# Performance work log

Hardware: AMD Instinct MI355X
Metric: run time of the kernel (lower is better)

Reference implementation:

```python
import jax, jax.numpy as jnp
import numpy as np

DIM = 1024
SCALE = 1.0 / np.sqrt(DIM).astype(np.float32)


def setup_inputs() -> dict:
    key = jax.random.key(0)
    ks = jax.random.split(key, 8)
    B, S, D = 4, 2048, DIM
    x = jax.random.normal(ks[0], (B, S, D), dtype=jnp.float32)
    mask = jnp.zeros((S, S), dtype=jnp.float32)  # additive mask, broadcast over batch
    # learned params (nn.Linear: y = x @ W.T + b); store W already transposed for x @ W
    init = 1.0 / np.sqrt(D)
    Wq = jax.random.uniform(ks[1], (D, D), jnp.float32, -init, init)
    bq = jax.random.uniform(ks[2], (D,), jnp.float32, -init, init)
    Wk = jax.random.uniform(ks[3], (D, D), jnp.float32, -init, init)
    bk = jax.random.uniform(ks[4], (D,), jnp.float32, -init, init)
    Wv = jax.random.uniform(ks[5], (D, D), jnp.float32, -init, init)
    bv = jax.random.uniform(ks[6], (D,), jnp.float32, -init, init)
    return {"x": x, "mask": mask, "Wq": Wq, "bq": bq, "Wk": Wk, "bk": bk, "Wv": Wv, "bv": bv}


def reference(x, mask, Wq, bq, Wk, bk, Wv, bv):
    # single-head full-dim attention, scaled by 1/sqrt(dim) (as in the source)
    q = x @ Wq + bq                      # [B, S, D]
    k = x @ Wk + bk                      # [B, S, D]
    v = x @ Wv + bv                      # [B, S, D]
    scores = jnp.einsum('bqd,bkd->bqk', q, k) * SCALE  # [B, S, S]
    scores = scores + mask               # additive mask, broadcast
    attn = jax.nn.softmax(scores, axis=-1)
    # dropout(p=0.1) is identity in eval mode
    return jnp.einsum('bqk,bkd->bqd', attn, v)  # [B, S, D]
```

## Files before the change

kernel.cpp:

```cpp
#include <hip/hip_runtime.h>

typedef unsigned short u16;
typedef unsigned int u32;

typedef __attribute__((ext_vector_type(8))) short bf16x8;
typedef __attribute__((ext_vector_type(4))) float f32x4;

static __device__ __forceinline__ u16 f2bf(float f) {
    u32 u = __float_as_uint(f);
    u32 r = (u + 0x7FFFu + ((u >> 16) & 1u)) >> 16;
    return (u16)r;
}
static __device__ __forceinline__ float bf2f(u16 h) {
    return __uint_as_float(((u32)h) << 16);
}
static __device__ __forceinline__ u32 pack2(float a, float b) {
    return (u32)f2bf(a) | ((u32)f2bf(b) << 16);
}

__global__ __launch_bounds__(256) void convert_bf16_kernel(const float* __restrict__ x,
                                                           u16* __restrict__ y, int n4) {
    int i = blockIdx.x * 256 + threadIdx.x;
    if (i < n4) {
        float4 v = ((const float4*)x)[i];
        ushort4 o;
        o.x = f2bf(v.x); o.y = f2bf(v.y); o.z = f2bf(v.z); o.w = f2bf(v.w);
        ((ushort4*)y)[i] = o;
    }
}

__global__ __launch_bounds__(256) void transpose_to_bf16_kernel(const float* __restrict__ W,
                                                                u16* __restrict__ WT, int D) {
    __shared__ float t[32][33];
    int bx = blockIdx.x, by = blockIdx.y;
    int tx = threadIdx.x, ty = threadIdx.y;
#pragma unroll
    for (int i = ty; i < 32; i += 8)
        t[i][tx] = W[(long)(by * 32 + i) * D + bx * 32 + tx];
    __syncthreads();
#pragma unroll
    for (int i = ty; i < 32; i += 8)
        WT[(long)(bx * 32 + i) * D + by * 32 + tx] = f2bf(t[tx][i]);
}

__global__ __launch_bounds__(256) void concat_bias_kernel(const float* __restrict__ a,
                                                          const float* __restrict__ b,
                                                          float* __restrict__ o, int n) {
    int i = blockIdx.x * 256 + threadIdx.x;
    if (i < 2 * n) o[i] = (i < n) ? a[i] : b[i - n];
}


__global__ __launch_bounds__(512, 4) void gemm_wide_kernel(
    const u16* __restrict__ A, int lda, long sA,
    const u16* __restrict__ B, int ldb, long sB,
    void* __restrict__ C, int ldc, long sC, int c_bf16,
    const float* __restrict__ bias, int bias_mode,
    const float* __restrict__ madd, int mask_ld,
    float scale, int K) {
    __shared__ __align__(16) u16 SMEM[2][384 * 32];
    const int bz = blockIdx.z;
    const u16* Ab = A + (long)bz * sA;
    const u16* Bb = B + (long)bz * sB;
    const int tm = blockIdx.y * 256, tn = blockIdx.x * 128;
    const int tid = threadIdx.x, wave = tid >> 6, lane = tid & 63;
    const int wm = (wave & 3) * 64, wn = (wave >> 2) * 64;
    const int lr = lane >> 2, c = lane & 3;
    const int fm = lane & 15, fq = lane >> 4;

    f32x4 acc[4][4];
#pragma unroll
    for (int i = 0; i < 4; i++)
#pragma unroll
        for (int j = 0; j < 4; j++) acc[i][j] = (f32x4){0.f, 0.f, 0.f, 0.f};

    const int T = K >> 5;

    auto stage = [&](int t, int buf) {
        u16* As = &SMEM[buf][0];
        u16* Bs = &SMEM[buf][256 * 32];
#pragma unroll
        for (int r = 0; r < 2; r++) {
            const int rl = wave * 32 + r * 16;
            const int row = rl + lr;
            const int kc = (t << 5) + ((c ^ ((row ^ (row >> 2)) & 3)) << 3);
            const u16* ga = Ab + (long)(tm + row) * lda + kc;
            __builtin_amdgcn_global_load_lds((const __attribute__((address_space(1))) void*)ga,
                                             (__attribute__((address_space(3))) void*)&As[rl * 32],
                                             16, 0, 0);
        }
        {
            const int rl = wave * 16;
            const int row = rl + lr;
            const int kc = (t << 5) + ((c ^ ((row ^ (row >> 2)) & 3)) << 3);
            const u16* gb = Bb + (long)(tn + row) * ldb + kc;
            __builtin_amdgcn_global_load_lds((const __attribute__((address_space(1))) void*)gb,
                                             (__attribute__((address_space(3))) void*)&Bs[rl * 32],
                                             16, 0, 0);
        }
    };

    stage(0, 0);
    __syncthreads();
    for (int t = 0; t < T; t++) {
        const int cur = t & 1;
        if (t + 1 < T) stage(t + 1, cur ^ 1);
        const u16* As = &SMEM[cur][0];
        const u16* Bs = &SMEM[cur][256 * 32];
        bf16x8 af[4], bfr[4];
#pragma unroll
        for (int i = 0; i < 4; i++) {
            int row = wm + i * 16 + fm;
            af[i] = *(const bf16x8*)&As[row * 32 + ((fq ^ ((row ^ (row >> 2)) & 3)) << 3)];
        }
#pragma unroll
        for (int j = 0; j < 4; j++) {
            int row = wn + j * 16 + fm;
            bfr[j] = *(const bf16x8*)&Bs[row * 32 + ((fq ^ ((row ^ (row >> 2)) & 3)) << 3)];
        }
#pragma unroll
        for (int i = 0; i < 4; i++)
#pragma unroll
            for (int j = 0; j < 4; j++)
                acc[i][j] = __builtin_amdgcn_mfma_f32_16x16x32_bf16(af[i], bfr[j], acc[i][j], 0, 0, 0);
        if (t + 1 < T) __syncthreads();
    }
    __syncthreads();

    float* EP = (float*)&SMEM[0][0] + wave * 1088;
    const int row16 = lane >> 2, cb = (lane & 3) * 16;
    float4 bc[4];
    if (bias_mode == 1) {
#pragma unroll
        for (int q = 0; q < 4; q++) bc[q] = *(const float4*)&bias[tn + wn + cb + q * 4];
    }
#pragma unroll
    for (int i = 0; i < 4; i++) {
#pragma unroll
        for (int j = 0; j < 4; j++)
#pragma unroll
            for (int r = 0; r < 4; r++)
                EP[(fq * 4 + r) * 68 + j * 16 + fm] = acc[i][j][r];
        const long grow = tm + wm + i * 16 + row16;
        float rb = (bias_mode == 2) ? bias[grow] : 0.f;
        float4 t4[4];
#pragma unroll
        for (int q = 0; q < 4; q++) {
            float4 v = *(const float4*)&EP[row16 * 68 + cb + q * 4];
            v.x = v.x * scale + rb; v.y = v.y * scale + rb;
            v.z = v.z * scale + rb; v.w = v.w * scale + rb;
            if (bias_mode == 1) { v.x += bc[q].x; v.y += bc[q].y; v.z += bc[q].z; v.w += bc[q].w; }
            if (madd) {
                float4 m4 = *(const float4*)&madd[grow * mask_ld + tn + wn + cb + q * 4];
                v.x += m4.x; v.y += m4.y; v.z += m4.z; v.w += m4.w;
            }
            t4[q] = v;
        }
        if (c_bf16) {
            u16* dst = (u16*)C + (long)bz * sC + grow * ldc + tn + wn + cb;
            uint4 o0 = {pack2(t4[0].x, t4[0].y), pack2(t4[0].z, t4[0].w),
                        pack2(t4[1].x, t4[1].y), pack2(t4[1].z, t4[1].w)};
            uint4 o1 = {pack2(t4[2].x, t4[2].y), pack2(t4[2].z, t4[2].w),
                        pack2(t4[3].x, t4[3].y), pack2(t4[3].z, t4[3].w)};
            *(uint4*)dst = o0;
            *(uint4*)(dst + 8) = o1;
        } else {
            float* dst = (float*)C + (long)bz * sC + grow * ldc + tn + wn + cb;
#pragma unroll
            for (int q = 0; q < 4; q++) *(float4*)(dst + q * 4) = t4[q];
        }
    }
}

__global__ __launch_bounds__(256, 4) void gemm_bt_kernel(
    const u16* __restrict__ A, int lda, long sA,
    const u16* __restrict__ B, int ldb, long sB,
    void* __restrict__ C, int ldc, long sC, int c_bf16,
    const float* __restrict__ bias, int bias_mode,
    const float* __restrict__ madd, int mask_ld,
    float scale, int K) {
    __shared__ __align__(16) u16 SMEM[2][256 * 32];
    const int bz = blockIdx.z;
    const u16* Ab = A + (long)bz * sA;
    const u16* Bb = B + (long)bz * sB;
    const int tm = blockIdx.y * 128, tn = blockIdx.x * 128;
    const int tid = threadIdx.x, wave = tid >> 6, lane = tid & 63;
    const int wm = (wave >> 1) * 64, wn = (wave & 1) * 64;
    const int lr = lane >> 2, c = lane & 3;
    const int fm = lane & 15, fq = lane >> 4;

    f32x4 acc[4][4];
#pragma unroll
    for (int i = 0; i < 4; i++)
#pragma unroll
        for (int j = 0; j < 4; j++) acc[i][j] = (f32x4){0.f, 0.f, 0.f, 0.f};

    const int T = K >> 5;

    auto stage = [&](int t, int buf) {
        u16* As = &SMEM[buf][0];
        u16* Bs = &SMEM[buf][128 * 32];
#pragma unroll
        for (int r = 0; r < 2; r++) {
            const int rl = r * 64 + wave * 16;
            const int row = rl + lr;
            const int kc = (t << 5) + ((c ^ ((row ^ (row >> 2)) & 3)) << 3);
            const u16* ga = Ab + (long)(tm + row) * lda + kc;
            const u16* gb = Bb + (long)(tn + row) * ldb + kc;
            __builtin_amdgcn_global_load_lds((const __attribute__((address_space(1))) void*)ga,
                                             (__attribute__((address_space(3))) void*)&As[rl * 32],
                                             16, 0, 0);
            __builtin_amdgcn_global_load_lds((const __attribute__((address_space(1))) void*)gb,
                                             (__attribute__((address_space(3))) void*)&Bs[rl * 32],
                                             16, 0, 0);
        }
    };

    stage(0, 0);
    __syncthreads();
    for (int t = 0; t < T; t++) {
        const int cur = t & 1;
        if (t + 1 < T) stage(t + 1, cur ^ 1);
        const u16* As = &SMEM[cur][0];
        const u16* Bs = &SMEM[cur][128 * 32];
        bf16x8 af[4], bfr[4];
#pragma unroll
        for (int i = 0; i < 4; i++) {
            int row = wm + i * 16 + fm;
            af[i] = *(const bf16x8*)&As[row * 32 + ((fq ^ ((row ^ (row >> 2)) & 3)) << 3)];
        }
#pragma unroll
        for (int j = 0; j < 4; j++) {
            int row = wn + j * 16 + fm;
            bfr[j] = *(const bf16x8*)&Bs[row * 32 + ((fq ^ ((row ^ (row >> 2)) & 3)) << 3)];
        }
#pragma unroll
        for (int i = 0; i < 4; i++)
#pragma unroll
            for (int j = 0; j < 4; j++)
                acc[i][j] = __builtin_amdgcn_mfma_f32_16x16x32_bf16(af[i], bfr[j], acc[i][j], 0, 0, 0);
        if (t + 1 < T) __syncthreads();
    }
    __syncthreads();

    float* EP = (float*)&SMEM[0][0] + wave * 1088;
    const int row16 = lane >> 2, cb = (lane & 3) * 16;
    float4 bc[4];
    if (bias_mode == 1) {
#pragma unroll
        for (int q = 0; q < 4; q++) bc[q] = *(const float4*)&bias[tn + wn + cb + q * 4];
    }
#pragma unroll
    for (int i = 0; i < 4; i++) {
#pragma unroll
        for (int j = 0; j < 4; j++)
#pragma unroll
            for (int r = 0; r < 4; r++)
                EP[(fq * 4 + r) * 68 + j * 16 + fm] = acc[i][j][r];
        const long grow = tm + wm + i * 16 + row16;
        float rb = (bias_mode == 2) ? bias[grow] : 0.f;
        float4 t4[4];
#pragma unroll
        for (int q = 0; q < 4; q++) {
            float4 v = *(const float4*)&EP[row16 * 68 + cb + q * 4];
            v.x = v.x * scale + rb; v.y = v.y * scale + rb;
            v.z = v.z * scale + rb; v.w = v.w * scale + rb;
            if (bias_mode == 1) { v.x += bc[q].x; v.y += bc[q].y; v.z += bc[q].z; v.w += bc[q].w; }
            if (madd) {
                float4 m4 = *(const float4*)&madd[grow * mask_ld + tn + wn + cb + q * 4];
                v.x += m4.x; v.y += m4.y; v.z += m4.z; v.w += m4.w;
            }
            t4[q] = v;
        }
        if (c_bf16) {
            u16* dst = (u16*)C + (long)bz * sC + grow * ldc + tn + wn + cb;
            uint4 o0 = {pack2(t4[0].x, t4[0].y), pack2(t4[0].z, t4[0].w),
                        pack2(t4[1].x, t4[1].y), pack2(t4[1].z, t4[1].w)};
            uint4 o1 = {pack2(t4[2].x, t4[2].y), pack2(t4[2].z, t4[2].w),
                        pack2(t4[3].x, t4[3].y), pack2(t4[3].z, t4[3].w)};
            *(uint4*)dst = o0;
            *(uint4*)(dst + 8) = o1;
        } else {
            float* dst = (float*)C + (long)bz * sC + grow * ldc + tn + wn + cb;
#pragma unroll
            for (int q = 0; q < 4; q++) *(float4*)(dst + q * 4) = t4[q];
        }
    }
}

__global__ __launch_bounds__(256) void softmax_kernel(u16* __restrict__ s) {
    const long row = blockIdx.x;
    u16* p = s + row * 2048;
    const int tid = threadIdx.x;
    const int lane = tid & 63, wave = tid >> 6;
    __shared__ float redm[4], reds[4];

    uint4 raw = ((const uint4*)p)[tid];
    float v[8];
    v[0] = bf2f(raw.x & 0xffff); v[1] = bf2f(raw.x >> 16);
    v[2] = bf2f(raw.y & 0xffff); v[3] = bf2f(raw.y >> 16);
    v[4] = bf2f(raw.z & 0xffff); v[5] = bf2f(raw.z >> 16);
    v[6] = bf2f(raw.w & 0xffff); v[7] = bf2f(raw.w >> 16);

    float m = v[0];
#pragma unroll
    for (int k = 1; k < 8; k++) m = fmaxf(m, v[k]);
#pragma unroll
    for (int off = 32; off; off >>= 1) m = fmaxf(m, __shfl_xor(m, off));
    if (lane == 0) redm[wave] = m;
    __syncthreads();
    m = fmaxf(fmaxf(redm[0], redm[1]), fmaxf(redm[2], redm[3]));

    float sum = 0.f;
#pragma unroll
    for (int k = 0; k < 8; k++) { v[k] = __expf(v[k] - m); sum += v[k]; }
#pragma unroll
    for (int off = 32; off; off >>= 1) sum += __shfl_xor(sum, off);
    if (lane == 0) reds[wave] = sum;
    __syncthreads();
    sum = reds[0] + reds[1] + reds[2] + reds[3];
    float inv = 1.f / sum;

    uint4 o;
    o.x = pack2(v[0] * inv, v[1] * inv);
    o.y = pack2(v[2] * inv, v[3] * inv);
    o.z = pack2(v[4] * inv, v[5] * inv);
    o.w = pack2(v[6] * inv, v[7] * inv);
    ((uint4*)p)[tid] = o;
}

extern "C" void kernel_launch(void* const* d_in, const int* in_sizes, int n_in,
                              void* d_out, int out_size, void* d_ws, size_t ws_size,
                              hipStream_t stream) {
    const float* x    = (const float*)d_in[0];
    const float* mask = (const float*)d_in[1];
    const float* Wq   = (const float*)d_in[2];
    const float* bq   = (const float*)d_in[3];
    const float* Wk   = (const float*)d_in[4];
    const float* bk   = (const float*)d_in[5];
    const float* Wv   = (const float*)d_in[6];
    const float* bv   = (const float*)d_in[7];
    float* out = (float*)d_out;

    const int B = 4, S = 2048, D = 1024;
    const long MS = (long)B * S;

    size_t need = (size_t)MS * D * 2 + (size_t)(2 * D) * D * 2 + (size_t)D * D * 2
                + (size_t)(2 * D) * 4 + (size_t)MS * (2 * D) * 2 + (size_t)D * MS * 2
                + (size_t)B * S * S * 2;
    if (ws_size < need) return;

    char* ws = (char*)d_ws;
    u16*  xb   = (u16*)ws;  ws += (long)MS * D * 2;
    u16*  wqkt = (u16*)ws;  ws += (long)(2 * D) * D * 2;
    u16*  wvt  = (u16*)ws;  ws += (long)D * D * 2;
    float* bqk = (float*)ws; ws += (long)(2 * D) * 4;
    u16*  QK   = (u16*)ws;  ws += (long)MS * (2 * D) * 2;
    u16*  VT   = (u16*)ws;  ws += (long)D * MS * 2;
    u16*  sc   = (u16*)ws;  ws += (long)B * S * S * 2;

    const float SCALE = 0.03125f;

    convert_bf16_kernel<<<(int)((MS * D / 4 + 255) / 256), 256, 0, stream>>>(x, xb, (int)(MS * D / 4));
    dim3 tb(32, 8);
    transpose_to_bf16_kernel<<<dim3(32, 32), tb, 0, stream>>>(Wq, wqkt, D);
    transpose_to_bf16_kernel<<<dim3(32, 32), tb, 0, stream>>>(Wk, wqkt + (long)D * D, D);
    transpose_to_bf16_kernel<<<dim3(32, 32), tb, 0, stream>>>(Wv, wvt, D);
    concat_bias_kernel<<<8, 256, 0, stream>>>(bq, bk, bqk, D);

    gemm_wide_kernel<<<dim3(2 * D / 128, (int)(MS / 256), 1), 512, 0, stream>>>(
        xb, D, 0, wqkt, D, 0, QK, 2 * D, 0, 1, bqk, 1, nullptr, 0, 1.0f, D);
    gemm_bt_kernel<<<dim3((int)(MS / 128), D / 128, 1), 256, 0, stream>>>(
        wvt, D, 0, xb, D, 0, VT, (int)MS, 0, 1, bv, 2, nullptr, 0, 1.0f, D);

    gemm_wide_kernel<<<dim3(S / 128, S / 256, B), 512, 0, stream>>>(
        QK, 2 * D, (long)S * 2 * D, QK + D, 2 * D, (long)S * 2 * D, sc, S, (long)S * S, 1,
        nullptr, 0, mask, S, SCALE, D);

    softmax_kernel<<<B * S, 256, 0, stream>>>(sc);

    gemm_bt_kernel<<<dim3(D / 128, S / 128, B), 256, 0, stream>>>(
        sc, S, (long)S * S, VT, (int)MS, (long)S, out, D, (long)S * D, 0,
        nullptr, 0, nullptr, 0, 1.0f, S);
}
```

Baseline: 297.8 us.

## Load B fragments directly from global into registers, stage only A in LDS

Both GEMM kernels stop staging the B tile through shared memory. Each wave now loads its B MFMA fragments straight from global memory into registers, double-buffered across two register sets, while A keeps the LDS double buffer. The main loop is unrolled by two so the ping-pong buffers use static names. This cuts LDS footprint and LDS read traffic, but B loads become per-wave, uncoalesced 16-byte reads with more register pressure, so the occupancy hints drop to 2 and 3 blocks per CU.

```diff
diff --git a/kernel.cpp b/kernel.cpp
--- a/kernel.cpp
+++ b/kernel.cpp
@@ -51,14 +51,16 @@
 }
 
 
-__global__ __launch_bounds__(512, 4) void gemm_wide_kernel(
+__global__ __launch_bounds__(512, 2) void gemm_wide_kernel(
     const u16* __restrict__ A, int lda, long sA,
     const u16* __restrict__ B, int ldb, long sB,
     void* __restrict__ C, int ldc, long sC, int c_bf16,
     const float* __restrict__ bias, int bias_mode,
     const float* __restrict__ madd, int mask_ld,
     float scale, int K) {
-    __shared__ __align__(16) u16 SMEM[2][384 * 32];
+    __shared__ __align__(16) char SM[34816];
+    u16* A0 = (u16*)SM;
+    u16* A1 = (u16*)(SM + 16384);
     const int bz = blockIdx.z;
     const u16* Ab = A + (long)bz * sA;
     const u16* Bb = B + (long)bz * sB;
@@ -76,9 +78,7 @@
 
     const int T = K >> 5;
 
-    auto stage = [&](int t, int buf) {
-        u16* As = &SMEM[buf][0];
-        u16* Bs = &SMEM[buf][256 * 32];
+    auto stageA = [&](int t, u16* As) {
 #pragma unroll
         for (int r = 0; r < 2; r++) {
             const int rl = wave * 32 + r * 16;
@@ -89,45 +89,49 @@
                                              (__attribute__((address_space(3))) void*)&As[rl * 32],
                                              16, 0, 0);
         }
-        {
-            const int rl = wave * 16;
-            const int row = rl + lr;
-            const int kc = (t << 5) + ((c ^ ((row ^ (row >> 2)) & 3)) << 3);
-            const u16* gb = Bb + (long)(tn + row) * ldb + kc;
-            __builtin_amdgcn_global_load_lds((const __attribute__((address_space(1))) void*)gb,
-                                             (__attribute__((address_space(3))) void*)&Bs[rl * 32],
-                                             16, 0, 0);
-        }
-    };
-
-    stage(0, 0);
-    __syncthreads();
-    for (int t = 0; t < T; t++) {
-        const int cur = t & 1;
-        if (t + 1 < T) stage(t + 1, cur ^ 1);
-        const u16* As = &SMEM[cur][0];
-        const u16* Bs = &SMEM[cur][256 * 32];
-        bf16x8 af[4], bfr[4];
+    };
+    const u16* gb0 = Bb + (long)(tn + wn + 0 + fm) * ldb + fq * 8;
+    const u16* gb1 = Bb + (long)(tn + wn + 16 + fm) * ldb + fq * 8;
+    const u16* gb2 = Bb + (long)(tn + wn + 32 + fm) * ldb + fq * 8;
+    const u16* gb3 = Bb + (long)(tn + wn + 48 + fm) * ldb + fq * 8;
+    auto loadB = [&](int t, bf16x8 (&fb)[4]) {
+        const int ko = t << 5;
+        fb[0] = *(const bf16x8*)(gb0 + ko);
+        fb[1] = *(const bf16x8*)(gb1 + ko);
+        fb[2] = *(const bf16x8*)(gb2 + ko);
+        fb[3] = *(const bf16x8*)(gb3 + ko);
+    };
+    auto ldA = [&](const u16* As, bf16x8 (&af)[4]) {
 #pragma unroll
         for (int i = 0; i < 4; i++) {
             int row = wm + i * 16 + fm;
             af[i] = *(const bf16x8*)&As[row * 32 + ((fq ^ ((row ^ (row >> 2)) & 3)) << 3)];
         }
-#pragma unroll
-        for (int j = 0; j < 4; j++) {
-            int row = wn + j * 16 + fm;
-            bfr[j] = *(const bf16x8*)&Bs[row * 32 + ((fq ^ ((row ^ (row >> 2)) & 3)) << 3)];
-        }
+    };
+    auto domfma = [&](bf16x8 (&af)[4], bf16x8 (&fb)[4]) {
 #pragma unroll
         for (int i = 0; i < 4; i++)
 #pragma unroll
             for (int j = 0; j < 4; j++)
-                acc[i][j] = __builtin_amdgcn_mfma_f32_16x16x32_bf16(af[i], bfr[j], acc[i][j], 0, 0, 0);
+                acc[i][j] = __builtin_amdgcn_mfma_f32_16x16x32_bf16(af[i], fb[j], acc[i][j], 0, 0, 0);
+    };
+
+    bf16x8 fb0[4], fb1[4], af[4];
+    stageA(0, A0);
+    loadB(0, fb0);
+    __syncthreads();
+    for (int t = 0; t < T; t += 2) {
+        if (t + 1 < T) { stageA(t + 1, A1); loadB(t + 1, fb1); }
+        ldA(A0, af);
+        domfma(af, fb0);
         if (t + 1 < T) __syncthreads();
-    }
-    __syncthreads();
-
-    float* EP = (float*)&SMEM[0][0] + wave * 1088;
+        if (t + 2 < T) { stageA(t + 2, A0); loadB(t + 2, fb0); }
+        if (t + 1 < T) { ldA(A1, af); domfma(af, fb1); }
+        if (t + 2 < T) __syncthreads();
+    }
+    __syncthreads();
+
+    float* EP = (float*)SM + wave * 1088;
     const int row16 = lane >> 2, cb = (lane & 3) * 16;
     float4 bc[4];
     if (bias_mode == 1) {
@@ -172,14 +176,16 @@
     }
 }
 
-__global__ __launch_bounds__(256, 4) void gemm_bt_kernel(
+__global__ __launch_bounds__(256, 3) void gemm_bt_kernel(
     const u16* __restrict__ A, int lda, long sA,
     const u16* __restrict__ B, int ldb, long sB,
     void* __restrict__ C, int ldc, long sC, int c_bf16,
     const float* __restrict__ bias, int bias_mode,
     const float* __restrict__ madd, int mask_ld,
     float scale, int K) {
-    __shared__ __align__(16) u16 SMEM[2][256 * 32];
+    __shared__ __align__(16) char SM[17408];
+    u16* A0 = (u16*)SM;
+    u16* A1 = (u16*)(SM + 8192);
     const int bz = blockIdx.z;
     const u16* Ab = A + (long)bz * sA;
     const u16* Bb = B + (long)bz * sB;
@@ -197,53 +203,60 @@
 
     const int T = K >> 5;
 
-    auto stage = [&](int t, int buf) {
-        u16* As = &SMEM[buf][0];
-        u16* Bs = &SMEM[buf][128 * 32];
+    auto stageA = [&](int t, u16* As) {
 #pragma unroll
         for (int r = 0; r < 2; r++) {
             const int rl = r * 64 + wave * 16;
             const int row = rl + lr;
             const int kc = (t << 5) + ((c ^ ((row ^ (row >> 2)) & 3)) << 3);
             const u16* ga = Ab + (long)(tm + row) * lda + kc;
-            const u16* gb = Bb + (long)(tn + row) * ldb + kc;
             __builtin_amdgcn_global_load_lds((const __attribute__((address_space(1))) void*)ga,
                                              (__attribute__((address_space(3))) void*)&As[rl * 32],
                                              16, 0, 0);
-            __builtin_amdgcn_global_load_lds((const __attribute__((address_space(1))) void*)gb,
-                                             (__attribute__((address_space(3))) void*)&Bs[rl * 32],
-                                             16, 0, 0);
-        }
-    };
-
-    stage(0, 0);
-    __syncthreads();
-    for (int t = 0; t < T; t++) {
-        const int cur = t & 1;
-        if (t + 1 < T) stage(t + 1, cur ^ 1);
-        const u16* As = &SMEM[cur][0];
-        const u16* Bs = &SMEM[cur][128 * 32];
-        bf16x8 af[4], bfr[4];
+        }
+    };
+    const u16* gb0 = Bb + (long)(tn + wn + 0 + fm) * ldb + fq * 8;
+    const u16* gb1 = Bb + (long)(tn + wn + 16 + fm) * ldb + fq * 8;
+    const u16* gb2 = Bb + (long)(tn + wn + 32 + fm) * ldb + fq * 8;
+    const u16* gb3 = Bb + (long)(tn + wn + 48 + fm) * ldb + fq * 8;
+    auto loadB = [&](int t, bf16x8 (&fb)[4]) {
+        const int ko = t << 5;
+        fb[0] = *(const bf16x8*)(gb0 + ko);
+        fb[1] = *(const bf16x8*)(gb1 + ko);
+        fb[2] = *(const bf16x8*)(gb2 + ko);
+        fb[3] = *(const bf16x8*)(gb3 + ko);
+    };
+    auto ldA = [&](const u16* As, bf16x8 (&af)[4]) {
 #pragma unroll
         for (int i = 0; i < 4; i++) {
             int row = wm + i * 16 + fm;
             af[i] = *(const bf16x8*)&As[row * 32 + ((fq ^ ((row ^ (row >> 2)) & 3)) << 3)];
         }
-#pragma unroll
-        for (int j = 0; j < 4; j++) {
-            int row = wn + j * 16 + fm;
-            bfr[j] = *(const bf16x8*)&Bs[row * 32 + ((fq ^ ((row ^ (row >> 2)) & 3)) << 3)];
-        }
+    };
+    auto domfma = [&](bf16x8 (&af)[4], bf16x8 (&fb)[4]) {
 #pragma unroll
         for (int i = 0; i < 4; i++)
 #pragma unroll
             for (int j = 0; j < 4; j++)
-                acc[i][j] = __builtin_amdgcn_mfma_f32_16x16x32_bf16(af[i], bfr[j], acc[i][j], 0, 0, 0);
+                acc[i][j] = __builtin_amdgcn_mfma_f32_16x16x32_bf16(af[i], fb[j], acc[i][j], 0, 0, 0);
+    };
+
+    bf16x8 fb0[4], fb1[4], af[4];
+    stageA(0, A0);
+    loadB(0, fb0);
+    __syncthreads();
+    for (int t = 0; t < T; t += 2) {
+        if (t + 1 < T) { stageA(t + 1, A1); loadB(t + 1, fb1); }
+        ldA(A0, af);
+        domfma(af, fb0);
         if (t + 1 < T) __syncthreads();
-    }
-    __syncthreads();
-
-    float* EP = (float*)&SMEM[0][0] + wave * 1088;
+        if (t + 2 < T) { stageA(t + 2, A0); loadB(t + 2, fb0); }
+        if (t + 1 < T) { ldA(A1, af); domfma(af, fb1); }
+        if (t + 2 < T) __syncthreads();
+    }
+    __syncthreads();
+
+    float* EP = (float*)SM + wave * 1088;
     const int row16 = lane >> 2, cb = (lane & 3) * 16;
     float4 bc[4];
     if (bias_mode == 1) {
```

After: 454.4 us. 52.6% more time.
